# Kernel tuning notes

Hardware: AMD Instinct MI355X
Metric: run time of the kernel (lower is better)

Reference implementation:

```python
import jax, jax.numpy as jnp
import numpy as np

# dims: N patches, D_IN input feats, D model, DI=inner, DS=state, DC=conv, DTR=dt_rank
N, D_IN, D, DI, DS, DC, DTR, NC, NL = 4096, 1024, 512, 1024, 16, 4, 32, 4, 2


def setup_inputs() -> dict:
    key = jax.random.key(0)
    ks = jax.random.split(key, 16)
    g = lambda i, shape, s=0.02: jax.random.normal(ks[i], shape, dtype=jnp.float32) * s
    return {
        "data_s": jax.random.normal(ks[0], (N, 512), dtype=jnp.float32),
        "data_l": jax.random.normal(ks[1], (N, 512), dtype=jnp.float32),
        "coord_s": jax.random.uniform(ks[2], (N, 2), dtype=jnp.float32) * 1000.0,
        "label": jax.random.randint(ks[3], (1,), 0, NC),
        "fc1_w": g(4, (D, D_IN)), "fc1_b": jnp.zeros((D,), jnp.float32),
        "ln_w": jnp.ones((NL, D), jnp.float32), "ln_b": jnp.zeros((NL, D), jnp.float32),
        "in_proj_w": g(5, (NL, 2 * DI, D)),
        "conv_w": g(6, (NL, DI, DC), 0.1), "conv_b": jnp.zeros((NL, DI), jnp.float32),
        "x_proj_w": g(7, (NL, DTR + 2 * DS, DI)),
        "dt_proj_w": g(8, (NL, DI, DTR), 0.1), "dt_proj_b": g(9, (NL, DI), 0.5),
        "A_log": jnp.broadcast_to(jnp.log(jnp.arange(1, DS + 1, dtype=jnp.float32)), (NL, DI, DS)) + jnp.zeros((NL, DI, DS), jnp.float32),
        "D_param": jnp.ones((NL, DI), jnp.float32),
        "out_proj_w": g(10, (NL, D, DI)),
        "norm_w": jnp.ones((D,), jnp.float32), "norm_b": jnp.zeros((D,), jnp.float32),
        "attn_w1": g(11, (128, D)), "attn_b1": jnp.zeros((128,), jnp.float32),
        "attn_w2": g(12, (1, 128)), "attn_b2": jnp.zeros((1,), jnp.float32),
        "cls_w": g(13, (NC, D)), "cls_b": jnp.zeros((NC,), jnp.float32),
    }


def _layer_norm(x, w, b, eps=1e-5):
    m = x.mean(-1, keepdims=True)
    v = ((x - m) ** 2).mean(-1, keepdims=True)
    return (x - m) * jax.lax.rsqrt(v + eps) * w + b


def _mamba(h, inw, cw, cb, xpw, dtw, dtb, Alog, Dp, ow):
    # h: (B, L, D) -> (B, L, D); canonical Mamba block (mamba_ssm defaults)
    B, L, _ = h.shape
    xz = h @ inw.T                      # (B, L, 2*DI)
    x, z = jnp.split(xz, 2, axis=-1)
    # causal depthwise conv1d, kernel DC, left pad DC-1 (== torch pad+truncate)
    xp = jnp.pad(x, ((0, 0), (DC - 1, 0), (0, 0)))
    x = sum(xp[:, k:k + L, :] * cw[:, k] for k in range(DC)) + cb
    x = jax.nn.silu(x)
    xdbl = x @ xpw.T                    # (B, L, DTR + 2*DS)
    dt, Bm, Cm = jnp.split(xdbl, [DTR, DTR + DS], axis=-1)
    dt = jax.nn.softplus(dt @ dtw.T + dtb)   # (B, L, DI)
    A = -jnp.exp(Alog)                  # (DI, DS)
    dA = jnp.exp(dt[..., None] * A)                          # (B, L, DI, DS)
    dBx = dt[..., None] * Bm[:, :, None, :] * x[..., None]   # (B, L, DI, DS)

    def step(hst, inp):
        dA_t, dBx_t, C_t = inp
        hst = dA_t * hst + dBx_t        # (B, DI, DS)
        return hst, jnp.einsum('bds,bs->bd', hst, C_t)

    h0 = jnp.zeros((B, DI, DS), x.dtype)
    _, ys = jax.lax.scan(step, h0, (jnp.swapaxes(dA, 0, 1), jnp.swapaxes(dBx, 0, 1), jnp.swapaxes(Cm, 0, 1)))
    y = jnp.swapaxes(ys, 0, 1) + Dp * x
    return (y * jax.nn.silu(z)) @ ow.T


def _forward(data_s, data_l, coord_s, fc1_w, fc1_b, ln_w, ln_b, in_proj_w, conv_w, conv_b,
             x_proj_w, dt_proj_w, dt_proj_b, A_log, D_param, out_proj_w, norm_w, norm_b,
             attn_w1, attn_b1, attn_w2, attn_b2, cls_w, cls_b, label):
    h = jnp.concatenate([data_s, data_l], axis=1)            # (N, 1024)
    packed = jnp.concatenate([h, coord_s], axis=1)[None]     # (1, N, 1026)
    h = packed[:, :, :-2]                                    # strip coords
    h = jax.nn.relu(h @ fc1_w.T + fc1_b)                     # dropout: eval mode (identity)
    for i in range(NL):
        res = h
        hn = _layer_norm(h, ln_w[i], ln_b[i])
        h = _mamba(hn, in_proj_w[i], conv_w[i], conv_b[i], x_proj_w[i], dt_proj_w[i],
                   dt_proj_b[i], A_log[i], D_param[i], out_proj_w[i]) + res
    h = _layer_norm(h, norm_w, norm_b)
    A = jnp.tanh(h @ attn_w1.T + attn_b1) @ attn_w2.T + attn_b2   # (1, N, 1)
    A = jax.nn.softmax(jnp.swapaxes(A, 1, 2), axis=-1)            # (1, 1, N)
    hp = (A @ h)[0]                                               # (1, D)
    logits = hp @ cls_w.T + cls_b                                 # (1, NC)
    hz = jax.nn.sigmoid(logits)
    p = jnp.clip(hz, 1e-6, 1.0 - 1e-6)
    lce = jnp.log(p) - jnp.log1p(-p)                              # torch.logit
    Y_prob = jax.nn.softmax(lce, axis=1)
    loss = -jnp.take(jax.nn.log_softmax(lce, axis=1)[0], label[0])
    return lce, Y_prob, loss


def reference(data_s, data_l, coord_s, label, fc1_w, fc1_b, ln_w, ln_b, in_proj_w, conv_w,
              conv_b, x_proj_w, dt_proj_w, dt_proj_b, A_log, D_param, out_proj_w, norm_w,
              norm_b, attn_w1, attn_b1, attn_w2, attn_b2, cls_w, cls_b):
    return _forward(data_s, data_l, coord_s, fc1_w, fc1_b, ln_w, ln_b, in_proj_w, conv_w,
                    conv_b, x_proj_w, dt_proj_w, dt_proj_b, A_log, D_param, out_proj_w,
                    norm_w, norm_b, attn_w1, attn_b1, attn_w2, attn_b2, cls_w, cls_b, label)
```

## Files before the change

### kernel.cpp

```cpp
#include <hip/hip_runtime.h>
#include <math.h>

#define L_SEQ 4096
#define DMODEL 512
#define DIN    1024
#define DI     1024
#define DS     16
#define DC     4
#define DTR    32
#define NCHK   256
#define CL     16
#define SLAB   (L_SEQ * 64)

typedef __bf16 bf16x8 __attribute__((ext_vector_type(8)));
typedef __bf16 bf16x4 __attribute__((ext_vector_type(4)));
typedef float floatx4 __attribute__((ext_vector_type(4)));

__device__ __forceinline__ void gl2lds16(const __bf16* g, __bf16* l) {
    __builtin_amdgcn_global_load_lds(
        (const __attribute__((address_space(1))) void*)g,
        (__attribute__((address_space(3))) void*)l, 16, 0, 0);
}

template <int BN, int ACT, bool BIAS, bool ADDDEST, bool OUTBF, int KS>
__global__ __launch_bounds__(256) void gemm_mfma(
    const __bf16* __restrict__ A, int lda,
    const __bf16* __restrict__ W, int ldw,
    const float* __restrict__ bias,
    float* __restrict__ C, __bf16* __restrict__ Cb, int ldc, int K)
{
    __shared__ __align__(16) __bf16 sA[128 * 32];
    __shared__ __align__(16) __bf16 sB[BN * 32];
    const int tid = threadIdx.x;
    const int wid = tid >> 6, lane = tid & 63;
    const int m0 = blockIdx.y * 128;
    int n0;
    if (KS > 1) {
        const int ksl = blockIdx.x;
        A += (size_t)ksl * K;
        W += (size_t)ksl * K;
        C += (size_t)ksl * (size_t)gridDim.y * 128 * ldc;
        n0 = 0;
    } else {
        n0 = blockIdx.x * BN;
    }

    constexpr int MR = (BN == 128) ? 4 : 2;
    constexpr int NR = 4;
    const int wrow = (BN == 128) ? (wid >> 1) * 64 : wid * 32;
    const int wcol = (BN == 128) ? (wid & 1) * 64 : 0;

    const int srowA0 = wid * 32 + (lane >> 2);
    const int scol   = (lane & 3) * 8;
    const __bf16* aSrc0 = A + (size_t)(m0 + srowA0) * lda + scol;
    const __bf16* aSrc1 = aSrc0 + 16 * (size_t)lda;
    __bf16* aDst0 = &sA[wid * 1024];
    __bf16* aDst1 = &sA[wid * 1024 + 512];

    const __bf16* bSrc0;
    const __bf16* bSrc1 = nullptr;
    __bf16* bDst0;
    __bf16* bDst1 = nullptr;
    if (BN == 128) {
        bSrc0 = W + (size_t)(n0 + wid * 32 + (lane >> 2)) * ldw + scol;
        bSrc1 = bSrc0 + 16 * (size_t)ldw;
        bDst0 = &sB[wid * 1024];
        bDst1 = &sB[wid * 1024 + 512];
    } else {
        bSrc0 = W + (size_t)(n0 + wid * 16 + (lane >> 2)) * ldw + scol;
        bDst0 = &sB[wid * 512];
    }

    floatx4 acc[MR][NR] = {};
    const int fr = lane & 15;
    const int fk = (lane >> 4) * 8;

    for (int k0 = 0; k0 < K; k0 += 32) {
        __syncthreads();
        gl2lds16(aSrc0 + k0, aDst0);
        gl2lds16(aSrc1 + k0, aDst1);
        gl2lds16(bSrc0 + k0, bDst0);
        if (BN == 128) gl2lds16(bSrc1 + k0, bDst1);
        __syncthreads();
        bf16x8 af[MR], bfv[NR];
#pragma unroll
        for (int i = 0; i < MR; ++i)
            af[i] = *(const bf16x8*)&sA[(wrow + i * 16 + fr) * 32 + fk];
#pragma unroll
        for (int j = 0; j < NR; ++j)
            bfv[j] = *(const bf16x8*)&sB[(wcol + j * 16 + fr) * 32 + fk];
#pragma unroll
        for (int i = 0; i < MR; ++i)
#pragma unroll
            for (int j = 0; j < NR; ++j)
                acc[i][j] = __builtin_amdgcn_mfma_f32_16x16x32_bf16(
                    af[i], bfv[j], acc[i][j], 0, 0, 0);
    }

#pragma unroll
    for (int i = 0; i < MR; ++i)
#pragma unroll
        for (int j = 0; j < NR; ++j) {
            const int n = n0 + wcol + j * 16 + fr;
            float bv = 0.f;
            if (BIAS) bv = bias[n];
#pragma unroll
            for (int r = 0; r < 4; ++r) {
                const int m = m0 + wrow + i * 16 + (lane >> 4) * 4 + r;
                float v = acc[i][j][r] + bv;
                if (ACT == 1) v = fmaxf(v, 0.f);
                else if (ACT == 2) v = tanhf(v);
                const size_t idx = (size_t)m * ldc + n;
                if (OUTBF) {
                    Cb[idx] = (__bf16)v;
                } else {
                    if (ADDDEST) v += C[idx];
                    C[idx] = v;
                }
            }
        }
}

__global__ void f2b5_k(const float* __restrict__ s0, __bf16* __restrict__ d0, int n0,
                       const float* __restrict__ s1, __bf16* __restrict__ d1, int n1,
                       const float* __restrict__ s2, __bf16* __restrict__ d2, int n2,
                       const float* __restrict__ s3, __bf16* __restrict__ d3, int n3,
                       const float* __restrict__ s4, __bf16* __restrict__ d4, int n4)
{
    int i = blockIdx.x * 256 + threadIdx.x;
    const float* s; __bf16* d; int base;
    if (i < n0) { s = s0; d = d0; base = i; }
    else if (i < n0 + n1) { s = s1; d = d1; base = i - n0; }
    else if (i < n0 + n1 + n2) { s = s2; d = d2; base = i - n0 - n1; }
    else if (i < n0 + n1 + n2 + n3) { s = s3; d = d3; base = i - n0 - n1 - n2; }
    else if (i < n0 + n1 + n2 + n3 + n4) { s = s4; d = d4; base = i - n0 - n1 - n2 - n3; }
    else return;
    float4 a = ((const float4*)s)[2 * base], b = ((const float4*)s)[2 * base + 1];
    bf16x8 v;
    v[0] = (__bf16)a.x; v[1] = (__bf16)a.y; v[2] = (__bf16)a.z; v[3] = (__bf16)a.w;
    v[4] = (__bf16)b.x; v[5] = (__bf16)b.y; v[6] = (__bf16)b.z; v[7] = (__bf16)b.w;
    *(bf16x8*)&d[8 * base] = v;
}

__global__ void dtw_t_k(const float* __restrict__ src, float* __restrict__ dst)
{
    int i = blockIdx.x * 256 + threadIdx.x;
    int l = i >> 15, rem = i & 32767, r = rem >> 5, k = rem & 31;
    dst[l * 32768 + k * 1024 + r] = src[i];
}

__global__ void concat_bf_k(const float* __restrict__ a,
                            const float* __restrict__ b,
                            __bf16* __restrict__ o)
{
    int idx = blockIdx.x * 256 + threadIdx.x;
    int m = idx >> 7, c8 = (idx & 127) << 3;
    const float* src = (c8 < 512) ? &a[(m << 9) + c8] : &b[(m << 9) + c8 - 512];
    float4 x = ((const float4*)src)[0], y = ((const float4*)src)[1];
    bf16x8 v;
    v[0] = (__bf16)x.x; v[1] = (__bf16)x.y; v[2] = (__bf16)x.z; v[3] = (__bf16)x.w;
    v[4] = (__bf16)y.x; v[5] = (__bf16)y.y; v[6] = (__bf16)y.z; v[7] = (__bf16)y.w;
    *(bf16x8*)&o[idx << 3] = v;
}

template <int OMODE>
__global__ __launch_bounds__(128) void layernorm_k(
    const float* __restrict__ X, const float* __restrict__ w,
    const float* __restrict__ b, float* __restrict__ Yf, __bf16* __restrict__ Yb)
{
    const int r = blockIdx.x, tid = threadIdx.x;
    const size_t base = ((size_t)r << 9) + (tid << 2);
    const float4 v = *(const float4*)&X[base];
    float s = v.x + v.y + v.z + v.w;
#pragma unroll
    for (int o = 32; o; o >>= 1) s += __shfl_down(s, o, 64);
    __shared__ float red[2];
    if ((tid & 63) == 0) red[tid >> 6] = s;
    __syncthreads();
    const float mean = (red[0] + red[1]) * (1.f / 512.f);
    float dx = v.x - mean, dy = v.y - mean, dz = v.z - mean, dw = v.w - mean;
    float q = dx * dx + dy * dy + dz * dz + dw * dw;
#pragma unroll
    for (int o = 32; o; o >>= 1) q += __shfl_down(q, o, 64);
    __shared__ float red2[2];
    if ((tid & 63) == 0) red2[tid >> 6] = q;
    __syncthreads();
    const float rs = rsqrtf((red2[0] + red2[1]) * (1.f / 512.f) + 1e-5f);
    const float4 wv = *(const float4*)&w[tid << 2];
    const float4 bv = *(const float4*)&b[tid << 2];
    float o0 = dx * rs * wv.x + bv.x;
    float o1 = dy * rs * wv.y + bv.y;
    float o2 = dz * rs * wv.z + bv.z;
    float o3 = dw * rs * wv.w + bv.w;
    if (OMODE != 1) {
        float4 ov; ov.x = o0; ov.y = o1; ov.z = o2; ov.w = o3;
        *(float4*)&Yf[base] = ov;
    }
    if (OMODE != 0) {
        bf16x4 ov; ov[0] = (__bf16)o0; ov[1] = (__bf16)o1;
        ov[2] = (__bf16)o2; ov[3] = (__bf16)o3;
        *(bf16x4*)&Yb[base] = ov;
    }
}

__global__ void conv_silu_k(const __bf16* __restrict__ XZb,
                            const float* __restrict__ cw,
                            const float* __restrict__ cb,
                            __bf16* __restrict__ XCb)
{
    int i = blockIdx.x * 256 + threadIdx.x;
    int t = i >> 8, d4 = (i & 255) << 2;
    float wt[4][4];
#pragma unroll
    for (int d = 0; d < 4; ++d) {
        float4 w = *(const float4*)&cw[(d4 + d) << 2];
        wt[d][0] = w.x; wt[d][1] = w.y; wt[d][2] = w.z; wt[d][3] = w.w;
    }
    float4 c = *(const float4*)&cb[d4];
    float a0 = c.x, a1 = c.y, a2 = c.z, a3 = c.w;
#pragma unroll
    for (int k = 0; k < 4; ++k) {
        int ts = t + k - 3;
        if (ts >= 0) {
            bf16x4 x = *(const bf16x4*)&XZb[((size_t)ts << 11) + d4];
            a0 = fmaf((float)x[0], wt[0][k], a0);
            a1 = fmaf((float)x[1], wt[1][k], a1);
            a2 = fmaf((float)x[2], wt[2][k], a2);
            a3 = fmaf((float)x[3], wt[3][k], a3);
        }
    }
    a0 *= 1.f / (1.f + __expf(-a0));
    a1 *= 1.f / (1.f + __expf(-a1));
    a2 *= 1.f / (1.f + __expf(-a2));
    a3 *= 1.f / (1.f + __expf(-a3));
    bf16x4 ob; ob[0] = (__bf16)a0; ob[1] = (__bf16)a1;
    ob[2] = (__bf16)a2; ob[3] = (__bf16)a3;
    *(bf16x4*)&XCb[((size_t)t << 10) + d4] = ob;
}

__global__ __launch_bounds__(256) void scanA_k(
    const __bf16* __restrict__ xc, const float* __restrict__ xdblP,
    const float* __restrict__ dtwT, const float* __restrict__ dtb,
    const float* __restrict__ Alog,
    __bf16* __restrict__ sP, __bf16* __restrict__ sH)
{
    const int d = blockIdx.x * 256 + threadIdx.x;
    const int c = blockIdx.y;
    const int tid = threadIdx.x;
    __shared__ float xlow[CL][DTR];
    __shared__ float Bs[CL][DS];
#pragma unroll
    for (int u = 0; u < 2; ++u) {
        int idx = tid + u * 256;
        int t = idx >> 5, k = idx & 31;
        size_t g = (size_t)(c * CL + t) * 64 + k;
        xlow[t][k] = xdblP[g] + xdblP[SLAB + g] + xdblP[2 * SLAB + g] + xdblP[3 * SLAB + g];
    }
    {
        int t = tid >> 4, s = tid & 15;
        size_t g = (size_t)(c * CL + t) * 64 + 32 + s;
        Bs[t][s] = xdblP[g] + xdblP[SLAB + g] + xdblP[2 * SLAB + g] + xdblP[3 * SLAB + g];
    }
    __syncthreads();
    float dtw_d[32];
#pragma unroll
    for (int k = 0; k < 32; ++k) dtw_d[k] = dtwT[k * 1024 + d];
    const float dtb_d = dtb[d];
    float As[DS], h[DS];
    {
        const float4* Ap4 = (const float4*)&Alog[(size_t)d * DS];
#pragma unroll
        for (int q = 0; q < 4; ++q) {
            float4 a = Ap4[q];
            As[q * 4 + 0] = -__expf(a.x); As[q * 4 + 1] = -__expf(a.y);
            As[q * 4 + 2] = -__expf(a.z); As[q * 4 + 3] = -__expf(a.w);
        }
    }
#pragma unroll
    for (int s = 0; s < DS; ++s) h[s] = 0.f;
    float sumdt = 0.f;
    for (int t = 0; t < CL; ++t) {
        float acc = dtb_d;
#pragma unroll
        for (int k4 = 0; k4 < 8; ++k4) {
            float4 xq = *(const float4*)&xlow[t][k4 * 4];
            acc = fmaf(xq.x, dtw_d[k4 * 4 + 0], acc);
            acc = fmaf(xq.y, dtw_d[k4 * 4 + 1], acc);
            acc = fmaf(xq.z, dtw_d[k4 * 4 + 2], acc);
            acc = fmaf(xq.w, dtw_d[k4 * 4 + 3], acc);
        }
        float dtv = (acc > 20.f) ? acc : log1pf(__expf(acc));
        float xv = (float)xc[((size_t)(c * CL + t) << 10) + d];
        float dx = dtv * xv;
        sumdt += dtv;
        float barr[16];
#pragma unroll
        for (int q = 0; q < 4; ++q) {
            float4 b = *(const float4*)&Bs[t][q * 4];
            barr[q * 4 + 0] = b.x; barr[q * 4 + 1] = b.y;
            barr[q * 4 + 2] = b.z; barr[q * 4 + 3] = b.w;
        }
#pragma unroll
        for (int s = 0; s < DS; ++s) {
            float a = __expf(dtv * As[s]);
            h[s] = fmaf(a, h[s], dx * barr[s]);
        }
    }
    size_t base = ((size_t)c * DI + d) * DS;
    bf16x8 p0, p1, h0, h1;
#pragma unroll
    for (int s = 0; s < 8; ++s) {
        p0[s] = (__bf16)__expf(As[s] * sumdt);
        p1[s] = (__bf16)__expf(As[s + 8] * sumdt);
        h0[s] = (__bf16)h[s];
        h1[s] = (__bf16)h[s + 8];
    }
    *(bf16x8*)&sP[base] = p0; *(bf16x8*)&sP[base + 8] = p1;
    *(bf16x8*)&sH[base] = h0; *(bf16x8*)&sH[base + 8] = h1;
}

__global__ __launch_bounds__(64) void scanB_k(
    const __bf16* __restrict__ sP, const __bf16* __restrict__ sH,
    __bf16* __restrict__ Hin)
{
    int p = blockIdx.x * 64 + threadIdx.x;
    float run = 0.f;
#pragma unroll 4
    for (int c = 0; c < NCHK; ++c) {
        size_t idx = (size_t)c * DI * DS + p;
        Hin[idx] = (__bf16)run;
        run = fmaf((float)sP[idx], run, (float)sH[idx]);
    }
}

__global__ __launch_bounds__(256) void scanC_k(
    const __bf16* __restrict__ xc, const float* __restrict__ xdblP,
    const float* __restrict__ dtwT, const float* __restrict__ dtb,
    const float* __restrict__ Alog, const float* __restrict__ Dp,
    const __bf16* __restrict__ XZb, const __bf16* __restrict__ Hin,
    __bf16* __restrict__ yz)
{
    const int d = blockIdx.x * 256 + threadIdx.x;
    const int c = blockIdx.y;
    const int tid = threadIdx.x;
    __shared__ float xlow[CL][DTR];
    __shared__ float Bs[CL][DS], Cs[CL][DS];
#pragma unroll
    for (int u = 0; u < 2; ++u) {
        int idx = tid + u * 256;
        int t = idx >> 5, k = idx & 31;
        size_t g = (size_t)(c * CL + t) * 64 + k;
        xlow[t][k] = xdblP[g] + xdblP[SLAB + g] + xdblP[2 * SLAB + g] + xdblP[3 * SLAB + g];
    }
    {
        int t = tid >> 4, s = tid & 15;
        size_t g = (size_t)(c * CL + t) * 64 + 32 + s;
        Bs[t][s] = xdblP[g] + xdblP[SLAB + g] + xdblP[2 * SLAB + g] + xdblP[3 * SLAB + g];
        g += 16;
        Cs[t][s] = xdblP[g] + xdblP[SLAB + g] + xdblP[2 * SLAB + g] + xdblP[3 * SLAB + g];
    }
    __syncthreads();
    float dtw_d[32];
#pragma unroll
    for (int k = 0; k < 32; ++k) dtw_d[k] = dtwT[k * 1024 + d];
    const float dtb_d = dtb[d];
    float As[DS], h[DS];
    {
        const float4* Ap4 = (const float4*)&Alog[(size_t)d * DS];
#pragma unroll
        for (int q = 0; q < 4; ++q) {
            float4 a = Ap4[q];
            As[q * 4 + 0] = -__expf(a.x); As[q * 4 + 1] = -__expf(a.y);
            As[q * 4 + 2] = -__expf(a.z); As[q * 4 + 3] = -__expf(a.w);
        }
    }
    {
        size_t hbase = ((size_t)c * DI + d) * DS;
        bf16x8 h0 = *(const bf16x8*)&Hin[hbase];
        bf16x8 h1 = *(const bf16x8*)&Hin[hbase + 8];
#pragma unroll
        for (int s = 0; s < 8; ++s) { h[s] = (float)h0[s]; h[s + 8] = (float)h1[s]; }
    }
    const float Dd = Dp[d];
    for (int t = 0; t < CL; ++t) {
        float acc = dtb_d;
#pragma unroll
        for (int k4 = 0; k4 < 8; ++k4) {
            float4 xq = *(const float4*)&xlow[t][k4 * 4];
            acc = fmaf(xq.x, dtw_d[k4 * 4 + 0], acc);
            acc = fmaf(xq.y, dtw_d[k4 * 4 + 1], acc);
            acc = fmaf(xq.z, dtw_d[k4 * 4 + 2], acc);
            acc = fmaf(xq.w, dtw_d[k4 * 4 + 3], acc);
        }
        float dtv = (acc > 20.f) ? acc : log1pf(__expf(acc));
        size_t tg = (size_t)(c * CL + t);
        float xv = (float)xc[(tg << 10) + d];
        float dx = dtv * xv;
        float barr[16], carr[16];
#pragma unroll
        for (int q = 0; q < 4; ++q) {
            float4 b = *(const float4*)&Bs[t][q * 4];
            float4 cc = *(const float4*)&Cs[t][q * 4];
            barr[q * 4 + 0] = b.x; barr[q * 4 + 1] = b.y;
            barr[q * 4 + 2] = b.z; barr[q * 4 + 3] = b.w;
            carr[q * 4 + 0] = cc.x; carr[q * 4 + 1] = cc.y;
            carr[q * 4 + 2] = cc.z; carr[q * 4 + 3] = cc.w;
        }
        float y = 0.f;
#pragma unroll
        for (int s = 0; s < DS; ++s) {
            float a = __expf(dtv * As[s]);
            h[s] = fmaf(a, h[s], dx * barr[s]);
            y = fmaf(h[s], carr[s], y);
        }
        y = fmaf(Dd, xv, y);
        float zv = (float)XZb[(tg << 11) + 1024 + d];
        float sg = 1.f / (1.f + __expf(-zv));
        yz[(tg << 10) + d] = (__bf16)(y * (zv * sg));
    }
}

__global__ void score_k(const float* __restrict__ At,
                        const float* __restrict__ w2,
                        const float* __restrict__ b2,
                        float* __restrict__ sc)
{
    int t = blockIdx.x * 256 + threadIdx.x;
    const float4* a = (const float4*)(At + ((size_t)t << 7));
    const float4* w = (const float4*)w2;
    float acc = 0.f;
#pragma unroll
    for (int j = 0; j < 32; ++j) {
        float4 av = a[j], wv = w[j];
        acc += av.x * wv.x + av.y * wv.y + av.z * wv.z + av.w * wv.w;
    }
    sc[t] = acc + b2[0];
}

__global__ __launch_bounds__(256) void softmax_k(const float* __restrict__ s,
                                                 float* __restrict__ p)
{
    const int tid = threadIdx.x;
    float vals[16];
#pragma unroll
    for (int i = 0; i < 4; ++i) {
        float4 v = *(const float4*)&s[(tid << 4) + (i << 2)];
        vals[i * 4 + 0] = v.x; vals[i * 4 + 1] = v.y;
        vals[i * 4 + 2] = v.z; vals[i * 4 + 3] = v.w;
    }
    float mx = -1e30f;
#pragma unroll
    for (int i = 0; i < 16; ++i) mx = fmaxf(mx, vals[i]);
#pragma unroll
    for (int o = 32; o; o >>= 1) mx = fmaxf(mx, __shfl_xor(mx, o, 64));
    __shared__ float red[4];
    if ((tid & 63) == 0) red[tid >> 6] = mx;
    __syncthreads();
    mx = fmaxf(fmaxf(red[0], red[1]), fmaxf(red[2], red[3]));
    float sum = 0.f, e[16];
#pragma unroll
    for (int i = 0; i < 16; ++i) { e[i] = __expf(vals[i] - mx); sum += e[i]; }
#pragma unroll
    for (int o = 32; o; o >>= 1) sum += __shfl_xor(sum, o, 64);
    __syncthreads();
    if ((tid & 63) == 0) red[tid >> 6] = sum;
    __syncthreads();
    sum = red[0] + red[1] + red[2] + red[3];
    float inv = 1.f / sum;
#pragma unroll
    for (int i = 0; i < 4; ++i) {
        float4 ov;
        ov.x = e[i * 4 + 0] * inv; ov.y = e[i * 4 + 1] * inv;
        ov.z = e[i * 4 + 2] * inv; ov.w = e[i * 4 + 3] * inv;
        *(float4*)&p[(tid << 4) + (i << 2)] = ov;
    }
}

__global__ void pool_partial_k(const float* __restrict__ prob,
                               const float* __restrict__ hln,
                               float* __restrict__ part)
{
    int j = blockIdx.x * 256 + threadIdx.x;
    int c = blockIdx.y;
    float acc = 0.f;
    for (int t = c * 128; t < (c + 1) * 128; ++t)
        acc = fmaf(prob[t], hln[((size_t)t << 9) + j], acc);
    part[c * 512 + j] = acc;
}

__global__ void pool_reduce_k(const float* __restrict__ part,
                              float* __restrict__ hp)
{
    int j = blockIdx.x * 256 + threadIdx.x;
    float acc = 0.f;
    for (int c = 0; c < 32; ++c) acc += part[c * 512 + j];
    hp[j] = acc;
}

__global__ __launch_bounds__(256) void final_head_k(
    const float* __restrict__ hp, const float* __restrict__ cls_w,
    const float* __restrict__ cls_b, const int* __restrict__ label,
    float* __restrict__ out)
{
    const int w = threadIdx.x >> 6, lane = threadIdx.x & 63;
    float acc = 0.f;
    for (int k = lane; k < 512; k += 64) acc += hp[k] * cls_w[w * 512 + k];
#pragma unroll
    for (int o = 32; o; o >>= 1) acc += __shfl_down(acc, o, 64);
    __shared__ float lg[4];
    if (lane == 0) lg[w] = acc + cls_b[w];
    __syncthreads();
    if (threadIdx.x == 0) {
        float lce[4];
        for (int c = 0; c < 4; ++c) {
            float z = lg[c];
            float hz = 1.f / (1.f + expf(-z));
            float pc = fminf(fmaxf(hz, 1e-6f), 1.f - 1e-6f);
            lce[c] = logf(pc) - log1pf(-pc);
        }
        float mx = fmaxf(fmaxf(lce[0], lce[1]), fmaxf(lce[2], lce[3]));
        float se = 0.f;
        for (int c = 0; c < 4; ++c) se += expf(lce[c] - mx);
        for (int c = 0; c < 4; ++c) out[c] = lce[c];
        for (int c = 0; c < 4; ++c) out[4 + c] = expf(lce[c] - mx) / se;
        int lb = label[0];
        out[8] = -(lce[lb] - mx - logf(se));
    }
}

extern "C" void kernel_launch(void* const* d_in, const int* in_sizes, int n_in,
                              void* d_out, int out_size, void* d_ws, size_t ws_size,
                              hipStream_t stream)
{
    const float* data_s   = (const float*)d_in[0];
    const float* data_l   = (const float*)d_in[1];
    const int*   label    = (const int*)d_in[3];
    const float* fc1_w    = (const float*)d_in[4];
    const float* fc1_b    = (const float*)d_in[5];
    const float* ln_w     = (const float*)d_in[6];
    const float* ln_b     = (const float*)d_in[7];
    const float* in_proj_w= (const float*)d_in[8];
    const float* conv_w   = (const float*)d_in[9];
    const float* conv_b   = (const float*)d_in[10];
    const float* x_proj_w = (const float*)d_in[11];
    const float* dt_proj_w= (const float*)d_in[12];
    const float* dt_proj_b= (const float*)d_in[13];
    const float* A_log    = (const float*)d_in[14];
    const float* D_param  = (const float*)d_in[15];
    const float* out_proj_w=(const float*)d_in[16];
    const float* norm_w   = (const float*)d_in[17];
    const float* norm_b   = (const float*)d_in[18];
    const float* attn_w1  = (const float*)d_in[19];
    const float* attn_b1  = (const float*)d_in[20];
    const float* attn_w2  = (const float*)d_in[21];
    const float* attn_b2  = (const float*)d_in[22];
    const float* cls_w    = (const float*)d_in[23];
    const float* cls_b    = (const float*)d_in[24];
    float* out = (float*)d_out;

    float* ws = (float*)d_ws;
    size_t off = 0;
    float* h     = ws + off; off += (size_t)L_SEQ * DMODEL;
    float* hn    = ws + off; off += (size_t)L_SEQ * DMODEL;
    float* xdblP = ws + off; off += (size_t)4 * SLAB;
    float* dtwT  = ws + off; off += (size_t)2 * DTR * DI;
    float* At    = ws + off; off += (size_t)L_SEQ * 128;
    float* sc    = ws + off; off += L_SEQ;
    float* pb    = ws + off; off += L_SEQ;
    float* part  = ws + off; off += 32 * 512;
    float* hp    = ws + off; off += 512;

    __bf16* bws = (__bf16*)(ws + off);
    size_t boff = 0;
    __bf16* Acatb = bws + boff; boff += (size_t)L_SEQ * DIN;
    __bf16* hnb   = bws + boff; boff += (size_t)L_SEQ * DMODEL;
    __bf16* XZb   = bws + boff; boff += (size_t)L_SEQ * 2 * DI;
    __bf16* XCb   = bws + boff; boff += (size_t)L_SEQ * DI;
    __bf16* yzb   = bws + boff; boff += (size_t)L_SEQ * DI;
    __bf16* sPb   = bws + boff; boff += (size_t)NCHK * DI * DS;
    __bf16* sHb   = bws + boff; boff += (size_t)NCHK * DI * DS;
    __bf16* HinB  = bws + boff; boff += (size_t)NCHK * DI * DS;
    __bf16* wfc1b = bws + boff; boff += (size_t)DMODEL * DIN;
    __bf16* winb  = bws + boff; boff += (size_t)2 * 2 * DI * DMODEL;
    __bf16* wxpb  = bws + boff; boff += (size_t)2 * 64 * DI;
    __bf16* woutb = bws + boff; boff += (size_t)2 * DMODEL * DI;
    __bf16* w1b   = bws + boff; boff += (size_t)128 * DMODEL;
    if (ws_size < off * sizeof(float) + boff * sizeof(__bf16)) return;

    const int n0 = DMODEL * DIN / 8;
    const int n1 = 2 * 2 * DI * DMODEL / 8;
    const int n2 = 2 * 64 * DI / 8;
    const int n3 = 2 * DMODEL * DI / 8;
    const int n4 = 128 * DMODEL / 8;
    f2b5_k<<<(n0 + n1 + n2 + n3 + n4 + 255) / 256, 256, 0, stream>>>(
        fc1_w, wfc1b, n0, in_proj_w, winb, n1, x_proj_w, wxpb, n2,
        out_proj_w, woutb, n3, attn_w1, w1b, n4);
    dtw_t_k<<<2 * DI * DTR / 256, 256, 0, stream>>>(dt_proj_w, dtwT);

    concat_bf_k<<<L_SEQ * DIN / 8 / 256, 256, 0, stream>>>(data_s, data_l, Acatb);
    gemm_mfma<64, 1, true, false, false, 1><<<dim3(DMODEL / 64, L_SEQ / 128), 256, 0, stream>>>(
        Acatb, DIN, wfc1b, DIN, fc1_b, h, nullptr, DMODEL, DIN);

    for (int i = 0; i < 2; ++i) {
        const __bf16* inw = winb + (size_t)i * 2 * DI * DMODEL;
        const float* cwi = conv_w + (size_t)i * DI * DC;
        const float* cbi = conv_b + (size_t)i * DI;
        const __bf16* xpw = wxpb + (size_t)i * 64 * DI;
        const float* dtwTi = dtwT + (size_t)i * DTR * DI;
        const float* dtbv= dt_proj_b + (size_t)i * DI;
        const float* Alg = A_log + (size_t)i * DI * DS;
        const float* Dpi = D_param + (size_t)i * DI;
        const __bf16* owi = woutb + (size_t)i * DMODEL * DI;

        layernorm_k<1><<<L_SEQ, 128, 0, stream>>>(h, ln_w + i * DMODEL, ln_b + i * DMODEL, nullptr, hnb);
        gemm_mfma<128, 0, false, false, true, 1><<<dim3(2 * DI / 128, L_SEQ / 128), 256, 0, stream>>>(
            hnb, DMODEL, inw, DMODEL, nullptr, nullptr, XZb, 2 * DI, DMODEL);
        conv_silu_k<<<L_SEQ * DI / 4 / 256, 256, 0, stream>>>(XZb, cwi, cbi, XCb);
        gemm_mfma<64, 0, false, false, false, 4><<<dim3(4, L_SEQ / 128), 256, 0, stream>>>(
            XCb, DI, xpw, DI, nullptr, xdblP, nullptr, 64, DI / 4);
        scanA_k<<<dim3(DI / 256, NCHK), 256, 0, stream>>>(XCb, xdblP, dtwTi, dtbv, Alg, sPb, sHb);
        scanB_k<<<DI * DS / 64, 64, 0, stream>>>(sPb, sHb, HinB);
        scanC_k<<<dim3(DI / 256, NCHK), 256, 0, stream>>>(XCb, xdblP, dtwTi, dtbv, Alg, Dpi, XZb, HinB, yzb);
        gemm_mfma<64, 0, false, true, false, 1><<<dim3(DMODEL / 64, L_SEQ / 128), 256, 0, stream>>>(
            yzb, DI, owi, DI, nullptr, h, nullptr, DMODEL, DI);
    }

    layernorm_k<2><<<L_SEQ, 128, 0, stream>>>(h, norm_w, norm_b, hn, hnb);
    gemm_mfma<64, 2, true, false, false, 1><<<dim3(2, L_SEQ / 128), 256, 0, stream>>>(
        hnb, DMODEL, w1b, DMODEL, attn_b1, At, nullptr, 128, DMODEL);
    score_k<<<L_SEQ / 256, 256, 0, stream>>>(At, attn_w2, attn_b2, sc);
    softmax_k<<<1, 256, 0, stream>>>(sc, pb);
    pool_partial_k<<<dim3(2, 32), 256, 0, stream>>>(pb, hn, part);
    pool_reduce_k<<<2, 256, 0, stream>>>(part, hp);
    final_head_k<<<1, 256, 0, stream>>>(hp, cls_w, cls_b, label, out);
}
```

Baseline: 435.3 us.

## Split SSM state across two half-waves per channel in scan kernels

The chunked scan kernels (scanA/scanC) now assign each channel to two lanes, each owning 8 of the 16 state dimensions and half of the dt_rank dot product, combined with a cross-half shuffle. The grid doubles to DI/128 blocks per chunk. This lowers per-thread register use (dtw, A, h arrays halved) and exposes more parallelism to raise occupancy. In exchange it adds shuffles, duplicates the softplus and dt work in both halves, and leaves half the lanes idle for the output store in scanC.

```diff
diff --git a/kernel.cpp b/kernel.cpp
--- a/kernel.cpp
+++ b/kernel.cpp
@@ -244,9 +244,11 @@
     const float* __restrict__ Alog,
     __bf16* __restrict__ sP, __bf16* __restrict__ sH)
 {
-    const int d = blockIdx.x * 256 + threadIdx.x;
+    const int tid = threadIdx.x;
+    const int wv = tid >> 6, lane = tid & 63;
+    const int half = lane >> 5;
+    const int d = blockIdx.x * 128 + wv * 32 + (lane & 31);
     const int c = blockIdx.y;
-    const int tid = threadIdx.x;
     __shared__ float xlow[CL][DTR];
     __shared__ float Bs[CL][DS];
 #pragma unroll
@@ -262,61 +264,59 @@
         Bs[t][s] = xdblP[g] + xdblP[SLAB + g] + xdblP[2 * SLAB + g] + xdblP[3 * SLAB + g];
     }
     __syncthreads();
-    float dtw_d[32];
-#pragma unroll
-    for (int k = 0; k < 32; ++k) dtw_d[k] = dtwT[k * 1024 + d];
+    float dtw_d[16];
+#pragma unroll
+    for (int k = 0; k < 16; ++k) dtw_d[k] = dtwT[(half * 16 + k) * 1024 + d];
     const float dtb_d = dtb[d];
-    float As[DS], h[DS];
+    float As[8], h[8];
     {
-        const float4* Ap4 = (const float4*)&Alog[(size_t)d * DS];
-#pragma unroll
-        for (int q = 0; q < 4; ++q) {
-            float4 a = Ap4[q];
-            As[q * 4 + 0] = -__expf(a.x); As[q * 4 + 1] = -__expf(a.y);
-            As[q * 4 + 2] = -__expf(a.z); As[q * 4 + 3] = -__expf(a.w);
-        }
-    }
-#pragma unroll
-    for (int s = 0; s < DS; ++s) h[s] = 0.f;
+        const float4* Ap4 = (const float4*)&Alog[(size_t)d * DS + half * 8];
+        float4 a0 = Ap4[0], a1 = Ap4[1];
+        As[0] = -__expf(a0.x); As[1] = -__expf(a0.y);
+        As[2] = -__expf(a0.z); As[3] = -__expf(a0.w);
+        As[4] = -__expf(a1.x); As[5] = -__expf(a1.y);
+        As[6] = -__expf(a1.z); As[7] = -__expf(a1.w);
+    }
+#pragma unroll
+    for (int s = 0; s < 8; ++s) h[s] = 0.f;
     float sumdt = 0.f;
     for (int t = 0; t < CL; ++t) {
-        float acc = dtb_d;
-#pragma unroll
-        for (int k4 = 0; k4 < 8; ++k4) {
-            float4 xq = *(const float4*)&xlow[t][k4 * 4];
-            acc = fmaf(xq.x, dtw_d[k4 * 4 + 0], acc);
-            acc = fmaf(xq.y, dtw_d[k4 * 4 + 1], acc);
-            acc = fmaf(xq.z, dtw_d[k4 * 4 + 2], acc);
-            acc = fmaf(xq.w, dtw_d[k4 * 4 + 3], acc);
-        }
+        const float* xl = &xlow[t][half * 16];
+        float p0 = 0.f, p1 = 0.f, p2 = 0.f, p3 = 0.f;
+#pragma unroll
+        for (int k4 = 0; k4 < 4; ++k4) {
+            float4 xq = *(const float4*)&xl[k4 * 4];
+            p0 = fmaf(xq.x, dtw_d[k4 * 4 + 0], p0);
+            p1 = fmaf(xq.y, dtw_d[k4 * 4 + 1], p1);
+            p2 = fmaf(xq.z, dtw_d[k4 * 4 + 2], p2);
+            p3 = fmaf(xq.w, dtw_d[k4 * 4 + 3], p3);
+        }
+        float acc = (p0 + p1) + (p2 + p3);
+        acc += __shfl_xor(acc, 32, 64);
+        acc += dtb_d;
         float dtv = (acc > 20.f) ? acc : log1pf(__expf(acc));
         float xv = (float)xc[((size_t)(c * CL + t) << 10) + d];
         float dx = dtv * xv;
         sumdt += dtv;
-        float barr[16];
-#pragma unroll
-        for (int q = 0; q < 4; ++q) {
-            float4 b = *(const float4*)&Bs[t][q * 4];
-            barr[q * 4 + 0] = b.x; barr[q * 4 + 1] = b.y;
-            barr[q * 4 + 2] = b.z; barr[q * 4 + 3] = b.w;
-        }
-#pragma unroll
-        for (int s = 0; s < DS; ++s) {
+        const float* bp = &Bs[t][half * 8];
+        float4 b0 = *(const float4*)&bp[0];
+        float4 b1 = *(const float4*)&bp[4];
+        float barr[8] = {b0.x, b0.y, b0.z, b0.w, b1.x, b1.y, b1.z, b1.w};
+#pragma unroll
+        for (int s = 0; s < 8; ++s) {
             float a = __expf(dtv * As[s]);
             h[s] = fmaf(a, h[s], dx * barr[s]);
         }
     }
-    size_t base = ((size_t)c * DI + d) * DS;
-    bf16x8 p0, p1, h0, h1;
+    size_t base = ((size_t)c * DI + d) * DS + half * 8;
+    bf16x8 pv, hv;
 #pragma unroll
     for (int s = 0; s < 8; ++s) {
-        p0[s] = (__bf16)__expf(As[s] * sumdt);
-        p1[s] = (__bf16)__expf(As[s + 8] * sumdt);
-        h0[s] = (__bf16)h[s];
-        h1[s] = (__bf16)h[s + 8];
-    }
-    *(bf16x8*)&sP[base] = p0; *(bf16x8*)&sP[base + 8] = p1;
-    *(bf16x8*)&sH[base] = h0; *(bf16x8*)&sH[base + 8] = h1;
+        pv[s] = (__bf16)__expf(As[s] * sumdt);
+        hv[s] = (__bf16)h[s];
+    }
+    *(bf16x8*)&sP[base] = pv;
+    *(bf16x8*)&sH[base] = hv;
 }
 
 __global__ __launch_bounds__(64) void scanB_k(
@@ -340,9 +340,11 @@
     const __bf16* __restrict__ XZb, const __bf16* __restrict__ Hin,
     __bf16* __restrict__ yz)
 {
-    const int d = blockIdx.x * 256 + threadIdx.x;
+    const int tid = threadIdx.x;
+    const int wv = tid >> 6, lane = tid & 63;
+    const int half = lane >> 5;
+    const int d = blockIdx.x * 128 + wv * 32 + (lane & 31);
     const int c = blockIdx.y;
-    const int tid = threadIdx.x;
     __shared__ float xlow[CL][DTR];
     __shared__ float Bs[CL][DS], Cs[CL][DS];
 #pragma unroll
@@ -360,63 +362,65 @@
         Cs[t][s] = xdblP[g] + xdblP[SLAB + g] + xdblP[2 * SLAB + g] + xdblP[3 * SLAB + g];
     }
     __syncthreads();
-    float dtw_d[32];
-#pragma unroll
-    for (int k = 0; k < 32; ++k) dtw_d[k] = dtwT[k * 1024 + d];
+    float dtw_d[16];
+#pragma unroll
+    for (int k = 0; k < 16; ++k) dtw_d[k] = dtwT[(half * 16 + k) * 1024 + d];
     const float dtb_d = dtb[d];
-    float As[DS], h[DS];
+    float As[8], h[8];
     {
-        const float4* Ap4 = (const float4*)&Alog[(size_t)d * DS];
-#pragma unroll
-        for (int q = 0; q < 4; ++q) {
-            float4 a = Ap4[q];
-            As[q * 4 + 0] = -__expf(a.x); As[q * 4 + 1] = -__expf(a.y);
-            As[q * 4 + 2] = -__expf(a.z); As[q * 4 + 3] = -__expf(a.w);
-        }
+        const float4* Ap4 = (const float4*)&Alog[(size_t)d * DS + half * 8];
+        float4 a0 = Ap4[0], a1 = Ap4[1];
+        As[0] = -__expf(a0.x); As[1] = -__expf(a0.y);
+        As[2] = -__expf(a0.z); As[3] = -__expf(a0.w);
+        As[4] = -__expf(a1.x); As[5] = -__expf(a1.y);
+        As[6] = -__expf(a1.z); As[7] = -__expf(a1.w);
     }
     {
-        size_t hbase = ((size_t)c * DI + d) * DS;
-        bf16x8 h0 = *(const bf16x8*)&Hin[hbase];
-        bf16x8 h1 = *(const bf16x8*)&Hin[hbase + 8];
-#pragma unroll
-        for (int s = 0; s < 8; ++s) { h[s] = (float)h0[s]; h[s + 8] = (float)h1[s]; }
+        bf16x8 hv = *(const bf16x8*)&Hin[((size_t)c * DI + d) * DS + half * 8];
+#pragma unroll
+        for (int s = 0; s < 8; ++s) h[s] = (float)hv[s];
     }
     const float Dd = Dp[d];
     for (int t = 0; t < CL; ++t) {
-        float acc = dtb_d;
-#pragma unroll
-        for (int k4 = 0; k4 < 8; ++k4) {
-            float4 xq = *(const float4*)&xlow[t][k4 * 4];
-            acc = fmaf(xq.x, dtw_d[k4 * 4 + 0], acc);
-            acc = fmaf(xq.y, dtw_d[k4 * 4 + 1], acc);
-            acc = fmaf(xq.z, dtw_d[k4 * 4 + 2], acc);
-            acc = fmaf(xq.w, dtw_d[k4 * 4 + 3], acc);
-        }
+        const float* xl = &xlow[t][half * 16];
+        float p0 = 0.f, p1 = 0.f, p2 = 0.f, p3 = 0.f;
+#pragma unroll
+        for (int k4 = 0; k4 < 4; ++k4) {
+            float4 xq = *(const float4*)&xl[k4 * 4];
+            p0 = fmaf(xq.x, dtw_d[k4 * 4 + 0], p0);
+            p1 = fmaf(xq.y, dtw_d[k4 * 4 + 1], p1);
+            p2 = fmaf(xq.z, dtw_d[k4 * 4 + 2], p2);
+            p3 = fmaf(xq.w, dtw_d[k4 * 4 + 3], p3);
+        }
+        float acc = (p0 + p1) + (p2 + p3);
+        acc += __shfl_xor(acc, 32, 64);
+        acc += dtb_d;
         float dtv = (acc > 20.f) ? acc : log1pf(__expf(acc));
         size_t tg = (size_t)(c * CL + t);
         float xv = (float)xc[(tg << 10) + d];
         float dx = dtv * xv;
-        float barr[16], carr[16];
-#pragma unroll
-        for (int q = 0; q < 4; ++q) {
-            float4 b = *(const float4*)&Bs[t][q * 4];
-            float4 cc = *(const float4*)&Cs[t][q * 4];
-            barr[q * 4 + 0] = b.x; barr[q * 4 + 1] = b.y;
-            barr[q * 4 + 2] = b.z; barr[q * 4 + 3] = b.w;
-            carr[q * 4 + 0] = cc.x; carr[q * 4 + 1] = cc.y;
-            carr[q * 4 + 2] = cc.z; carr[q * 4 + 3] = cc.w;
-        }
+        const float* bp = &Bs[t][half * 8];
+        const float* cp = &Cs[t][half * 8];
+        float4 b0 = *(const float4*)&bp[0];
+        float4 b1 = *(const float4*)&bp[4];
+        float4 c0 = *(const float4*)&cp[0];
+        float4 c1 = *(const float4*)&cp[4];
+        float barr[8] = {b0.x, b0.y, b0.z, b0.w, b1.x, b1.y, b1.z, b1.w};
+        float carr[8] = {c0.x, c0.y, c0.z, c0.w, c1.x, c1.y, c1.z, c1.w};
         float y = 0.f;
 #pragma unroll
-        for (int s = 0; s < DS; ++s) {
+        for (int s = 0; s < 8; ++s) {
             float a = __expf(dtv * As[s]);
             h[s] = fmaf(a, h[s], dx * barr[s]);
             y = fmaf(h[s], carr[s], y);
         }
-        y = fmaf(Dd, xv, y);
-        float zv = (float)XZb[(tg << 11) + 1024 + d];
-        float sg = 1.f / (1.f + __expf(-zv));
-        yz[(tg << 10) + d] = (__bf16)(y * (zv * sg));
+        y += __shfl_xor(y, 32, 64);
+        if (half == 0) {
+            y = fmaf(Dd, xv, y);
+            float zv = (float)XZb[(tg << 11) + 1024 + d];
+            float sg = 1.f / (1.f + __expf(-zv));
+            yz[(tg << 10) + d] = (__bf16)(y * (zv * sg));
+        }
     }
 }
 
@@ -618,9 +622,9 @@
         conv_silu_k<<<L_SEQ * DI / 4 / 256, 256, 0, stream>>>(XZb, cwi, cbi, XCb);
         gemm_mfma<64, 0, false, false, false, 4><<<dim3(4, L_SEQ / 128), 256, 0, stream>>>(
             XCb, DI, xpw, DI, nullptr, xdblP, nullptr, 64, DI / 4);
-        scanA_k<<<dim3(DI / 256, NCHK), 256, 0, stream>>>(XCb, xdblP, dtwTi, dtbv, Alg, sPb, sHb);
+        scanA_k<<<dim3(DI / 128, NCHK), 256, 0, stream>>>(XCb, xdblP, dtwTi, dtbv, Alg, sPb, sHb);
         scanB_k<<<DI * DS / 64, 64, 0, stream>>>(sPb, sHb, HinB);
-        scanC_k<<<dim3(DI / 256, NCHK), 256, 0, stream>>>(XCb, xdblP, dtwTi, dtbv, Alg, Dpi, XZb, HinB, yzb);
+        scanC_k<<<dim3(DI / 128, NCHK), 256, 0, stream>>>(XCb, xdblP, dtwTi, dtbv, Alg, Dpi, XZb, HinB, yzb);
         gemm_mfma<64, 0, false, true, false, 1><<<dim3(DMODEL / 64, L_SEQ / 128), 256, 0, stream>>>(
             yzb, DI, owi, DI, nullptr, h, nullptr, DMODEL, DI);
     }
```

Result: slower. 493.8 us (+13.4%).

## Cache softplus dt from scan pass A in bf16 and reuse it in pass C

Applied to the files above, without the earlier changes.

Pass A of the chunked selective scan now writes its per-timestep softplus(dt) values to a new bf16 buffer. Pass C reads them back instead of reloading the dt_rank slice of x_proj, the transposed dt_proj weights, and redoing the 32-term dot product and softplus. Both passes also prefetch the per-chunk x (and z in pass C) values into registers before the sequential loop, and pass A splits the dot product into four partial accumulators. The cost is extra global write and read traffic for the dt buffer, and dt is now rounded to bf16 in pass C, which may change numerics slightly.

```diff
diff --git a/kernel.cpp b/kernel.cpp
--- a/kernel.cpp
+++ b/kernel.cpp
@@ -242,7 +242,8 @@
     const __bf16* __restrict__ xc, const float* __restrict__ xdblP,
     const float* __restrict__ dtwT, const float* __restrict__ dtb,
     const float* __restrict__ Alog,
-    __bf16* __restrict__ sP, __bf16* __restrict__ sH)
+    __bf16* __restrict__ sP, __bf16* __restrict__ sH,
+    __bf16* __restrict__ dtc)
 {
     const int d = blockIdx.x * 256 + threadIdx.x;
     const int c = blockIdx.y;
@@ -262,6 +263,10 @@
         Bs[t][s] = xdblP[g] + xdblP[SLAB + g] + xdblP[2 * SLAB + g] + xdblP[3 * SLAB + g];
     }
     __syncthreads();
+    float xvv[CL];
+#pragma unroll
+    for (int t = 0; t < CL; ++t)
+        xvv[t] = (float)xc[((size_t)(c * CL + t) << 10) + d];
     float dtw_d[32];
 #pragma unroll
     for (int k = 0; k < 32; ++k) dtw_d[k] = dtwT[k * 1024 + d];
@@ -279,19 +284,22 @@
 #pragma unroll
     for (int s = 0; s < DS; ++s) h[s] = 0.f;
     float sumdt = 0.f;
+    float dts[CL];
+#pragma unroll
     for (int t = 0; t < CL; ++t) {
-        float acc = dtb_d;
+        float p0 = 0.f, p1 = 0.f, p2 = 0.f, p3 = 0.f;
 #pragma unroll
         for (int k4 = 0; k4 < 8; ++k4) {
             float4 xq = *(const float4*)&xlow[t][k4 * 4];
-            acc = fmaf(xq.x, dtw_d[k4 * 4 + 0], acc);
-            acc = fmaf(xq.y, dtw_d[k4 * 4 + 1], acc);
-            acc = fmaf(xq.z, dtw_d[k4 * 4 + 2], acc);
-            acc = fmaf(xq.w, dtw_d[k4 * 4 + 3], acc);
-        }
+            p0 = fmaf(xq.x, dtw_d[k4 * 4 + 0], p0);
+            p1 = fmaf(xq.y, dtw_d[k4 * 4 + 1], p1);
+            p2 = fmaf(xq.z, dtw_d[k4 * 4 + 2], p2);
+            p3 = fmaf(xq.w, dtw_d[k4 * 4 + 3], p3);
+        }
+        float acc = ((p0 + p1) + (p2 + p3)) + dtb_d;
         float dtv = (acc > 20.f) ? acc : log1pf(__expf(acc));
-        float xv = (float)xc[((size_t)(c * CL + t) << 10) + d];
-        float dx = dtv * xv;
+        dts[t] = dtv;
+        float dx = dtv * xvv[t];
         sumdt += dtv;
         float barr[16];
 #pragma unroll
@@ -307,16 +315,19 @@
         }
     }
     size_t base = ((size_t)c * DI + d) * DS;
-    bf16x8 p0, p1, h0, h1;
+    bf16x8 p0v, p1v, h0v, h1v, d0v, d1v;
 #pragma unroll
     for (int s = 0; s < 8; ++s) {
-        p0[s] = (__bf16)__expf(As[s] * sumdt);
-        p1[s] = (__bf16)__expf(As[s + 8] * sumdt);
-        h0[s] = (__bf16)h[s];
-        h1[s] = (__bf16)h[s + 8];
-    }
-    *(bf16x8*)&sP[base] = p0; *(bf16x8*)&sP[base + 8] = p1;
-    *(bf16x8*)&sH[base] = h0; *(bf16x8*)&sH[base + 8] = h1;
+        p0v[s] = (__bf16)__expf(As[s] * sumdt);
+        p1v[s] = (__bf16)__expf(As[s + 8] * sumdt);
+        h0v[s] = (__bf16)h[s];
+        h1v[s] = (__bf16)h[s + 8];
+        d0v[s] = (__bf16)dts[s];
+        d1v[s] = (__bf16)dts[s + 8];
+    }
+    *(bf16x8*)&sP[base] = p0v; *(bf16x8*)&sP[base + 8] = p1v;
+    *(bf16x8*)&sH[base] = h0v; *(bf16x8*)&sH[base + 8] = h1v;
+    *(bf16x8*)&dtc[base] = d0v; *(bf16x8*)&dtc[base + 8] = d1v;
 }
 
 __global__ __launch_bounds__(64) void scanB_k(
@@ -335,7 +346,7 @@
 
 __global__ __launch_bounds__(256) void scanC_k(
     const __bf16* __restrict__ xc, const float* __restrict__ xdblP,
-    const float* __restrict__ dtwT, const float* __restrict__ dtb,
+    const __bf16* __restrict__ dtc,
     const float* __restrict__ Alog, const float* __restrict__ Dp,
     const __bf16* __restrict__ XZb, const __bf16* __restrict__ Hin,
     __bf16* __restrict__ yz)
@@ -343,15 +354,7 @@
     const int d = blockIdx.x * 256 + threadIdx.x;
     const int c = blockIdx.y;
     const int tid = threadIdx.x;
-    __shared__ float xlow[CL][DTR];
     __shared__ float Bs[CL][DS], Cs[CL][DS];
-#pragma unroll
-    for (int u = 0; u < 2; ++u) {
-        int idx = tid + u * 256;
-        int t = idx >> 5, k = idx & 31;
-        size_t g = (size_t)(c * CL + t) * 64 + k;
-        xlow[t][k] = xdblP[g] + xdblP[SLAB + g] + xdblP[2 * SLAB + g] + xdblP[3 * SLAB + g];
-    }
     {
         int t = tid >> 4, s = tid & 15;
         size_t g = (size_t)(c * CL + t) * 64 + 32 + s;
@@ -360,10 +363,20 @@
         Cs[t][s] = xdblP[g] + xdblP[SLAB + g] + xdblP[2 * SLAB + g] + xdblP[3 * SLAB + g];
     }
     __syncthreads();
-    float dtw_d[32];
-#pragma unroll
-    for (int k = 0; k < 32; ++k) dtw_d[k] = dtwT[k * 1024 + d];
-    const float dtb_d = dtb[d];
+    size_t base = ((size_t)c * DI + d) * DS;
+    float dts[CL], xvv[CL], zvv[CL];
+    {
+        bf16x8 dd0 = *(const bf16x8*)&dtc[base];
+        bf16x8 dd1 = *(const bf16x8*)&dtc[base + 8];
+#pragma unroll
+        for (int s = 0; s < 8; ++s) { dts[s] = (float)dd0[s]; dts[s + 8] = (float)dd1[s]; }
+    }
+#pragma unroll
+    for (int t = 0; t < CL; ++t) {
+        size_t tg = (size_t)(c * CL + t);
+        xvv[t] = (float)xc[(tg << 10) + d];
+        zvv[t] = (float)XZb[(tg << 11) + 1024 + d];
+    }
     float As[DS], h[DS];
     {
         const float4* Ap4 = (const float4*)&Alog[(size_t)d * DS];
@@ -375,27 +388,17 @@
         }
     }
     {
-        size_t hbase = ((size_t)c * DI + d) * DS;
-        bf16x8 h0 = *(const bf16x8*)&Hin[hbase];
-        bf16x8 h1 = *(const bf16x8*)&Hin[hbase + 8];
+        bf16x8 h0 = *(const bf16x8*)&Hin[base];
+        bf16x8 h1 = *(const bf16x8*)&Hin[base + 8];
 #pragma unroll
         for (int s = 0; s < 8; ++s) { h[s] = (float)h0[s]; h[s + 8] = (float)h1[s]; }
     }
     const float Dd = Dp[d];
+#pragma unroll
     for (int t = 0; t < CL; ++t) {
-        float acc = dtb_d;
-#pragma unroll
-        for (int k4 = 0; k4 < 8; ++k4) {
-            float4 xq = *(const float4*)&xlow[t][k4 * 4];
-            acc = fmaf(xq.x, dtw_d[k4 * 4 + 0], acc);
-            acc = fmaf(xq.y, dtw_d[k4 * 4 + 1], acc);
-            acc = fmaf(xq.z, dtw_d[k4 * 4 + 2], acc);
-            acc = fmaf(xq.w, dtw_d[k4 * 4 + 3], acc);
-        }
-        float dtv = (acc > 20.f) ? acc : log1pf(__expf(acc));
-        size_t tg = (size_t)(c * CL + t);
-        float xv = (float)xc[(tg << 10) + d];
-        float dx = dtv * xv;
+        const float dtv = dts[t];
+        const float xv = xvv[t];
+        const float dx = dtv * xv;
         float barr[16], carr[16];
 #pragma unroll
         for (int q = 0; q < 4; ++q) {
@@ -414,9 +417,9 @@
             y = fmaf(h[s], carr[s], y);
         }
         y = fmaf(Dd, xv, y);
-        float zv = (float)XZb[(tg << 11) + 1024 + d];
+        float zv = zvv[t];
         float sg = 1.f / (1.f + __expf(-zv));
-        yz[(tg << 10) + d] = (__bf16)(y * (zv * sg));
+        yz[((size_t)(c * CL + t) << 10) + d] = (__bf16)(y * (zv * sg));
     }
 }
 
@@ -580,6 +583,7 @@
     __bf16* sPb   = bws + boff; boff += (size_t)NCHK * DI * DS;
     __bf16* sHb   = bws + boff; boff += (size_t)NCHK * DI * DS;
     __bf16* HinB  = bws + boff; boff += (size_t)NCHK * DI * DS;
+    __bf16* dtcB  = bws + boff; boff += (size_t)NCHK * DI * CL;
     __bf16* wfc1b = bws + boff; boff += (size_t)DMODEL * DIN;
     __bf16* winb  = bws + boff; boff += (size_t)2 * 2 * DI * DMODEL;
     __bf16* wxpb  = bws + boff; boff += (size_t)2 * 64 * DI;
@@ -618,9 +622,9 @@
         conv_silu_k<<<L_SEQ * DI / 4 / 256, 256, 0, stream>>>(XZb, cwi, cbi, XCb);
         gemm_mfma<64, 0, false, false, false, 4><<<dim3(4, L_SEQ / 128), 256, 0, stream>>>(
             XCb, DI, xpw, DI, nullptr, xdblP, nullptr, 64, DI / 4);
-        scanA_k<<<dim3(DI / 256, NCHK), 256, 0, stream>>>(XCb, xdblP, dtwTi, dtbv, Alg, sPb, sHb);
+        scanA_k<<<dim3(DI / 256, NCHK), 256, 0, stream>>>(XCb, xdblP, dtwTi, dtbv, Alg, sPb, sHb, dtcB);
         scanB_k<<<DI * DS / 64, 64, 0, stream>>>(sPb, sHb, HinB);
-        scanC_k<<<dim3(DI / 256, NCHK), 256, 0, stream>>>(XCb, xdblP, dtwTi, dtbv, Alg, Dpi, XZb, HinB, yzb);
+        scanC_k<<<dim3(DI / 256, NCHK), 256, 0, stream>>>(XCb, xdblP, dtcB, Alg, Dpi, XZb, HinB, yzb);
         gemm_mfma<64, 0, false, true, false, 1><<<dim3(DMODEL / 64, L_SEQ / 128), 256, 0, stream>>>(
             yzb, DI, owi, DI, nullptr, h, nullptr, DMODEL, DI);
     }
```

Result: no change. 436.7 us (+0.3%).
